# Performance work log

Measured on AMD Instinct MI355X. Metric: run time of the kernel, lower is better.

## Reference

```python
import jax, jax.numpy as jnp
import numpy as np

N_NODES = 50000
N_EDGES = 800000
D = 128
E_DIM = 32
N_LAYERS = 4
BN_EPS = 1e-5


def setup_inputs() -> dict:
    key = jax.random.key(0)
    ks = jax.random.split(key, 9)
    return {
        "x": jax.random.normal(ks[0], (N_NODES, D), dtype=jnp.float32),
        "edge_attr": jax.random.normal(ks[1], (N_EDGES, E_DIM), dtype=jnp.float32),
        "edge_index": jax.random.randint(ks[2], (2, N_EDGES), 0, N_NODES, dtype=jnp.int64),
        "W_edge": jax.random.normal(ks[3], (N_LAYERS, E_DIM, D), dtype=jnp.float32) * 0.1,
        "b_edge": jnp.zeros((N_LAYERS, D), dtype=jnp.float32),
        "W1": jax.random.normal(ks[4], (N_LAYERS, D, D), dtype=jnp.float32) * 0.1,
        "b1": jnp.zeros((N_LAYERS, D), dtype=jnp.float32),
        "W2": jax.random.normal(ks[5], (N_LAYERS, D, D), dtype=jnp.float32) * 0.1,
        "b2": jnp.zeros((N_LAYERS, D), dtype=jnp.float32),
        "gamma": jnp.ones((N_LAYERS, D), dtype=jnp.float32),
        "beta": jnp.zeros((N_LAYERS, D), dtype=jnp.float32),
    }


def reference(x, edge_attr, edge_index, W_edge, b_edge, W1, b1, W2, b2, gamma, beta):
    src, dst = edge_index[0], edge_index[1]
    n = x.shape[0]
    for i in range(N_LAYERS):
        # GINEConv: message = ReLU(x_src + Lin(edge_attr)); scatter-add to dst
        e = edge_attr @ W_edge[i] + b_edge[i]            # [E, D]
        m = jax.nn.relu(x[src] + e)                      # [E, D]
        agg = jax.ops.segment_sum(m, dst, num_segments=n)  # [N, D]
        h = x + agg                                      # (1+eps)*x, eps=0
        # 2-layer MLP
        h = jax.nn.relu(h @ W1[i] + b1[i]) @ W2[i] + b2[i]
        # BatchNorm (training-mode batch stats, biased var) + ReLU; dropout off
        mean = h.mean(axis=0)
        var = h.var(axis=0)
        h = (h - mean) * jax.lax.rsqrt(var + BN_EPS) * gamma[i] + beta[i]
        x = jax.nn.relu(h)
    return x
```

## Files before the change

### kernel.cpp

```cpp
#include <hip/hip_runtime.h>

#define NN 50000
#define NE 800000
#define DD 128
#define ED 32
#define NL 4
#define BN_EPS 1e-5f
#define SCAN_B 1024
#define NB ((NN + SCAN_B - 1) / SCAN_B)
#define EB 128
#define MR 32

typedef __attribute__((ext_vector_type(8))) short bf16x8;
typedef __attribute__((ext_vector_type(4))) float f32x4;

__device__ __forceinline__ unsigned short f2bf(float f) {
    unsigned u = __float_as_uint(f);
    u += 0x7fffu + ((u >> 16) & 1u);
    return (unsigned short)(u >> 16);
}
__device__ __forceinline__ float bf2f(unsigned short h) {
    return __uint_as_float((unsigned)h << 16);
}

__global__ __launch_bounds__(256) void hist_kernel(
    const int* __restrict__ edst, int* __restrict__ deg)
{
    const int e = blockIdx.x * 256 + threadIdx.x;
    if (e < NE) atomicAdd(&deg[edst[e]], 1);
}

__global__ __launch_bounds__(256) void scan1_kernel(
    const int* __restrict__ deg, int* __restrict__ rowptr, int* __restrict__ bsum)
{
    __shared__ int sh[256];
    const int t = threadIdx.x, b = blockIdx.x;
    const int base = b * SCAN_B + t * 4;
    int v[4];
#pragma unroll
    for (int j = 0; j < 4; ++j) {
        const int idx = base + j;
        v[j] = (idx < NN) ? deg[idx] : 0;
    }
    sh[t] = v[0] + v[1] + v[2] + v[3];
    __syncthreads();
    for (int off = 1; off < 256; off <<= 1) {
        const int val = (t >= off) ? sh[t - off] : 0;
        __syncthreads();
        sh[t] += val;
        __syncthreads();
    }
    int p = (t == 0) ? 0 : sh[t - 1];
#pragma unroll
    for (int j = 0; j < 4; ++j) {
        const int idx = base + j;
        if (idx < NN) rowptr[idx] = p;
        p += v[j];
    }
    if (t == 255) bsum[b] = sh[255];
}

__global__ void scan2_kernel(int* __restrict__ bsum)
{
    if (threadIdx.x == 0) {
        int acc = 0;
        for (int i = 0; i < NB; ++i) { const int v = bsum[i]; bsum[i] = acc; acc += v; }
    }
}

__global__ __launch_bounds__(256) void scan3_kernel(
    int* __restrict__ rowptr, int* __restrict__ cursor, const int* __restrict__ bsum)
{
    const int idx = blockIdx.x * 256 + threadIdx.x;
    if (idx < NN) {
        const int v = rowptr[idx] + bsum[idx / SCAN_B];
        rowptr[idx] = v;
        cursor[idx] = v;
    }
    if (idx == 0) rowptr[NN] = NE;
}

__global__ __launch_bounds__(256) void scatter_idx_kernel(
    const int* __restrict__ edst, int* __restrict__ cursor, int* __restrict__ eid_perm)
{
    const int e = blockIdx.x * 256 + threadIdx.x;
    if (e < NE) {
        const int pos = atomicAdd(&cursor[edst[e]], 1);
        eid_perm[pos] = e;
    }
}

__global__ __launch_bounds__(256) void sdea_kernel(
    const int* __restrict__ eid_perm, const int* __restrict__ esrc,
    const int* __restrict__ edst, const float* __restrict__ ea,
    int2* __restrict__ sd_perm, unsigned short* __restrict__ ea_bf)
{
    const int tid = blockIdx.x * 256 + threadIdx.x;
    const int pos = tid >> 3, j = tid & 7;
    if (pos < NE) {
        const int e = eid_perm[pos];
        if (j == 0) sd_perm[pos] = make_int2(esrc[e], edst[e]);
        const float4 v = *(const float4*)&ea[(size_t)e * ED + j * 4];
        uint2 p;
        p.x = (unsigned)f2bf(v.x) | ((unsigned)f2bf(v.y) << 16);
        p.y = (unsigned)f2bf(v.z) | ((unsigned)f2bf(v.w) << 16);
        *(uint2*)&ea_bf[(size_t)pos * ED + j * 4] = p;
    }
    if (tid == 0) sd_perm[NE] = make_int2(0, -1);
}

__global__ __launch_bounds__(256) void x0conv_kernel(
    const float* __restrict__ x0, unsigned short* __restrict__ xbf)
{
    const size_t i = ((size_t)blockIdx.x * 256 + threadIdx.x) * 8;
    if (i >= (size_t)NN * DD) return;
    const float4 a = *(const float4*)&x0[i];
    const float4 b = *(const float4*)&x0[i + 4];
    uint4 o;
    o.x = (unsigned)f2bf(a.x) | ((unsigned)f2bf(a.y) << 16);
    o.y = (unsigned)f2bf(a.z) | ((unsigned)f2bf(a.w) << 16);
    o.z = (unsigned)f2bf(b.x) | ((unsigned)f2bf(b.y) << 16);
    o.w = (unsigned)f2bf(b.z) | ((unsigned)f2bf(b.w) << 16);
    *(uint4*)&xbf[i] = o;
}

__global__ __launch_bounds__(256) void wconv_kernel(
    const float* __restrict__ We, unsigned short* __restrict__ wtb)
{
    const int tid = blockIdx.x * 256 + threadIdx.x;
    if (tid < NL * DD * ED) {
        const int l = tid / (DD * ED);
        const int r = tid % (DD * ED);
        const int c = r / ED, k = r % ED;
        wtb[tid] = f2bf(We[(size_t)l * ED * DD + k * DD + c]);
    }
}

__global__ __launch_bounds__(256) void w12conv_kernel(
    const float* __restrict__ W1, const float* __restrict__ W2,
    unsigned short* __restrict__ w1t, unsigned short* __restrict__ w2t)
{
    const int tid = blockIdx.x * 256 + threadIdx.x;
    if (tid < NL * DD * DD) {
        const int l = tid / (DD * DD);
        const int r = tid % (DD * DD);
        const int n = r / DD, k = r % DD;
        const size_t s = (size_t)l * DD * DD + k * DD + n;
        w1t[tid] = f2bf(W1[s]);
        w2t[tid] = f2bf(W2[s]);
    }
}

__global__ __launch_bounds__(256, 5) void edge_mfma_kernel(
    const unsigned short* __restrict__ xbf,
    const unsigned short* __restrict__ eab,
    const int2* __restrict__ sd_perm,
    const unsigned short* __restrict__ wtb,
    const float* __restrict__ be,
    float* __restrict__ agg)
{
    __shared__ unsigned short msgl[EB * 128];
    const int t = threadIdx.x;
    const int wv = t >> 6, ln = t & 63;
    const int l15 = ln & 15, kb = ln >> 4;

    const int nwg = NE / EB;
    const int q = nwg >> 3, r = nwg & 7;
    const int xcd = blockIdx.x & 7, seq = blockIdx.x >> 3;
    const int wg = (xcd < r ? xcd * (q + 1) : r * (q + 1) + (xcd - r) * q) + seq;
    const int e0 = wg * EB;

    const int c0 = (2 * wv + 0) * 16 + l15;
    const int c1 = (2 * wv + 1) * 16 + l15;
    const bf16x8 bfr0 = *(const bf16x8*)&wtb[c0 * ED + kb * 8];
    const bf16x8 bfr1 = *(const bf16x8*)&wtb[c1 * ED + kb * 8];
    const float bv0 = be[c0], bv1 = be[c1];

#pragma unroll
    for (int eg = 0; eg < EB / 16; ++eg) {
        const int edge = eg * 16 + l15;
        const bf16x8 afr = *(const bf16x8*)&eab[(size_t)(e0 + edge) * ED + kb * 8];
        f32x4 z = {0.f, 0.f, 0.f, 0.f};
        const f32x4 d0 = __builtin_amdgcn_mfma_f32_16x16x32_bf16(afr, bfr0, z, 0, 0, 0);
        const f32x4 d1 = __builtin_amdgcn_mfma_f32_16x16x32_bf16(afr, bfr1, z, 0, 0, 0);
#pragma unroll
        for (int j = 0; j < 4; ++j) {
            const int mrow = eg * 16 + kb * 4 + j;
            const int sw = ((mrow >> 2) & 3) << 3;
            const int i0 = (((c0 >> 1) ^ sw) << 1) | (c0 & 1);
            const int i1 = (((c1 >> 1) ^ sw) << 1) | (c1 & 1);
            msgl[mrow * 128 + i0] = f2bf(d0[j] + bv0);
            msgl[mrow * 128 + i1] = f2bf(d1[j] + bv1);
        }
    }
    __syncthreads();

    const int lbase = wv * 32;
    const int2* sdp = &sd_perm[e0 + lbase];
    const int c2 = ln * 2;
    float2 acc = {0.f, 0.f};
    int seg_start = 0;
#pragma unroll 1
    for (int g = 0; g < 2; ++g) {
        const int gb = g * 16;
        int4 pr[8];
#pragma unroll
        for (int q2 = 0; q2 < 8; ++q2)
            pr[q2] = *(const int4*)&sdp[gb + 2 * q2];
        int srcs[16], dsts[17];
#pragma unroll
        for (int q2 = 0; q2 < 8; ++q2) {
            srcs[2 * q2] = pr[q2].x; srcs[2 * q2 + 1] = pr[q2].z;
            dsts[2 * q2] = pr[q2].y; dsts[2 * q2 + 1] = pr[q2].w;
        }
        dsts[16] = sdp[gb + 16].y;
        float2 xv[16];
#pragma unroll
        for (int q2 = 0; q2 < 16; ++q2) {
            const unsigned xu = *(const unsigned*)&xbf[(size_t)srcs[q2] * DD + c2];
            xv[q2].x = __uint_as_float(xu << 16);
            xv[q2].y = __uint_as_float(xu & 0xffff0000u);
        }
#pragma unroll
        for (int q2 = 0; q2 < 16; ++q2) {
            const int i = gb + q2;
            const int dw = ln ^ (((i >> 2) & 3) << 3);
            const unsigned mm = *(const unsigned*)&msgl[(lbase + i) * 128 + dw * 2];
            const float mlo = __uint_as_float(mm << 16);
            const float mhi = __uint_as_float(mm & 0xffff0000u);
            acc.x += fmaxf(xv[q2].x + mlo, 0.f);
            acc.y += fmaxf(xv[q2].y + mhi, 0.f);
            if (i == 31 || dsts[q2 + 1] != dsts[q2]) {
                float* ap = &agg[(size_t)dsts[q2] * DD + c2];
                if (seg_start > 0 && i < 31) {
                    *(float2*)ap = acc;
                } else {
                    unsafeAtomicAdd(ap + 0, acc.x);
                    unsafeAtomicAdd(ap + 1, acc.y);
                }
                acc.x = 0.f; acc.y = 0.f;
                seg_start = i + 1;
            }
        }
    }
}

__global__ __launch_bounds__(256, 5) void mlp_mfma_kernel(
    const unsigned short* __restrict__ xbf, const float* __restrict__ agg,
    float* __restrict__ h2out,
    const unsigned short* __restrict__ w1t,
    const unsigned short* __restrict__ w2t,
    const float* __restrict__ b1, const float* __restrict__ b2,
    float* __restrict__ bns)
{
    __shared__ unsigned short ah[MR * 128];
    __shared__ unsigned short al[MR * 128];
    __shared__ unsigned short bh[MR * 128];
    const int t = threadIdx.x;
    const int wv = t >> 6, ln = t & 63, l15 = ln & 15, kb = ln >> 4;
    const int r0 = blockIdx.x * MR;

#pragma unroll
    for (int p = 0; p < 2; ++p) {
        const int row = p * 16 + (t >> 4);
        const int gc = t & 15;
        const int grow = r0 + row;
        float v[8] = {0.f, 0.f, 0.f, 0.f, 0.f, 0.f, 0.f, 0.f};
        if (grow < NN) {
            const size_t g = (size_t)grow * DD + gc * 8;
            const uint4 xu = *(const uint4*)&xbf[g];
            const float4 ga = *(const float4*)&agg[g];
            const float4 gb4 = *(const float4*)&agg[g + 4];
            v[0] = __uint_as_float(xu.x << 16)          + ga.x;
            v[1] = __uint_as_float(xu.x & 0xffff0000u)  + ga.y;
            v[2] = __uint_as_float(xu.y << 16)          + ga.z;
            v[3] = __uint_as_float(xu.y & 0xffff0000u)  + ga.w;
            v[4] = __uint_as_float(xu.z << 16)          + gb4.x;
            v[5] = __uint_as_float(xu.z & 0xffff0000u)  + gb4.y;
            v[6] = __uint_as_float(xu.w << 16)          + gb4.z;
            v[7] = __uint_as_float(xu.w & 0xffff0000u)  + gb4.w;
        }
        unsigned hiw[4], low[4];
#pragma unroll
        for (int j = 0; j < 4; ++j) {
            const unsigned short h0 = f2bf(v[2 * j]);
            const unsigned short h1 = f2bf(v[2 * j + 1]);
            const unsigned short q0 = f2bf(v[2 * j] - bf2f(h0));
            const unsigned short q1 = f2bf(v[2 * j + 1] - bf2f(h1));
            hiw[j] = (unsigned)h0 | ((unsigned)h1 << 16);
            low[j] = (unsigned)q0 | ((unsigned)q1 << 16);
        }
        const int off = row * 128 + (gc ^ (row & 7)) * 8;
        *(uint4*)&ah[off] = *(uint4*)hiw;
        *(uint4*)&al[off] = *(uint4*)low;
    }

    bf16x8 w1f[2][4];
#pragma unroll
    for (int nt = 0; nt < 2; ++nt) {
        const int n = wv * 32 + nt * 16 + l15;
#pragma unroll
        for (int ks = 0; ks < 4; ++ks)
            w1f[nt][ks] = *(const bf16x8*)&w1t[n * DD + ks * 32 + kb * 8];
    }
    const int cA = wv * 32 + l15, cB = wv * 32 + 16 + l15;
    const float b1v[2] = {b1[cA], b1[cB]};
    const float b2v[2] = {b2[cA], b2[cB]};
    __syncthreads();

    f32x4 acc[2][2];
#pragma unroll
    for (int mt = 0; mt < 2; ++mt)
#pragma unroll
        for (int nt = 0; nt < 2; ++nt)
            acc[mt][nt] = (f32x4){0.f, 0.f, 0.f, 0.f};
#pragma unroll
    for (int ks = 0; ks < 4; ++ks) {
#pragma unroll
        for (int mt = 0; mt < 2; ++mt) {
            const int row = mt * 16 + l15;
            const int off = row * 128 + ((ks * 4 + kb) ^ (row & 7)) * 8;
            const bf16x8 afh = *(const bf16x8*)&ah[off];
            const bf16x8 afl = *(const bf16x8*)&al[off];
#pragma unroll
            for (int nt = 0; nt < 2; ++nt) {
                acc[mt][nt] = __builtin_amdgcn_mfma_f32_16x16x32_bf16(afh, w1f[nt][ks], acc[mt][nt], 0, 0, 0);
                acc[mt][nt] = __builtin_amdgcn_mfma_f32_16x16x32_bf16(afl, w1f[nt][ks], acc[mt][nt], 0, 0, 0);
            }
        }
    }

#pragma unroll
    for (int mt = 0; mt < 2; ++mt) {
#pragma unroll
        for (int nt = 0; nt < 2; ++nt) {
            const int col = wv * 32 + nt * 16 + l15;
#pragma unroll
            for (int j = 0; j < 4; ++j) {
                const int row = mt * 16 + kb * 4 + j;
                const float v = fmaxf(acc[mt][nt][j] + b1v[nt], 0.f);
                const int off = row * 128 + ((col >> 3) ^ (row & 7)) * 8 + (col & 7);
                bh[off] = f2bf(v);
            }
        }
    }

    bf16x8 w2f[2][4];
#pragma unroll
    for (int nt = 0; nt < 2; ++nt) {
        const int n = wv * 32 + nt * 16 + l15;
#pragma unroll
        for (int ks = 0; ks < 4; ++ks)
            w2f[nt][ks] = *(const bf16x8*)&w2t[n * DD + ks * 32 + kb * 8];
    }
    __syncthreads();

#pragma unroll
    for (int mt = 0; mt < 2; ++mt)
#pragma unroll
        for (int nt = 0; nt < 2; ++nt)
            acc[mt][nt] = (f32x4){0.f, 0.f, 0.f, 0.f};
#pragma unroll
    for (int ks = 0; ks < 4; ++ks) {
#pragma unroll
        for (int mt = 0; mt < 2; ++mt) {
            const int row = mt * 16 + l15;
            const int off = row * 128 + ((ks * 4 + kb) ^ (row & 7)) * 8;
            const bf16x8 afh = *(const bf16x8*)&bh[off];
#pragma unroll
            for (int nt = 0; nt < 2; ++nt)
                acc[mt][nt] = __builtin_amdgcn_mfma_f32_16x16x32_bf16(afh, w2f[nt][ks], acc[mt][nt], 0, 0, 0);
        }
    }

    float ps[2] = {0.f, 0.f}, pq[2] = {0.f, 0.f};
#pragma unroll
    for (int mt = 0; mt < 2; ++mt) {
#pragma unroll
        for (int nt = 0; nt < 2; ++nt) {
            const int col = wv * 32 + nt * 16 + l15;
#pragma unroll
            for (int j = 0; j < 4; ++j) {
                const int row = r0 + mt * 16 + kb * 4 + j;
                const float v = acc[mt][nt][j] + b2v[nt];
                if (row < NN) {
                    h2out[(size_t)row * DD + col] = v;
                    ps[nt] += v;
                    pq[nt] += v * v;
                }
            }
        }
    }
#pragma unroll
    for (int nt = 0; nt < 2; ++nt) {
        ps[nt] += __shfl_xor(ps[nt], 16);
        ps[nt] += __shfl_xor(ps[nt], 32);
        pq[nt] += __shfl_xor(pq[nt], 16);
        pq[nt] += __shfl_xor(pq[nt], 32);
    }
    if (kb == 0) {
#pragma unroll
        for (int nt = 0; nt < 2; ++nt) {
            const int col = wv * 32 + nt * 16 + l15;
            unsafeAtomicAdd(&bns[col], ps[nt]);
            unsafeAtomicAdd(&bns[DD + col], pq[nt]);
        }
    }
}

__global__ __launch_bounds__(256) void bn_apply_bf16(
    float* __restrict__ h2, const float* __restrict__ bns,
    const float* __restrict__ gamma, const float* __restrict__ beta,
    unsigned short* __restrict__ xout)
{
    const size_t i = ((size_t)blockIdx.x * 256 + threadIdx.x) * 4;
    if (i >= (size_t)NN * DD) return;
    const int c4 = (int)(i & 127);
    const float4 hv = *(const float4*)&h2[i];
    const float4 sv = *(const float4*)&bns[c4];
    const float4 qv = *(const float4*)&bns[DD + c4];
    const float4 gv = *(const float4*)&gamma[c4];
    const float4 bv = *(const float4*)&beta[c4];
    const float inv_n = 1.f / (float)NN;
    float o0, o1, o2, o3;
    { const float m = sv.x * inv_n; const float var = qv.x * inv_n - m * m;
      o0 = fmaxf((hv.x - m) * __frsqrt_rn(var + BN_EPS) * gv.x + bv.x, 0.f); }
    { const float m = sv.y * inv_n; const float var = qv.y * inv_n - m * m;
      o1 = fmaxf((hv.y - m) * __frsqrt_rn(var + BN_EPS) * gv.y + bv.y, 0.f); }
    { const float m = sv.z * inv_n; const float var = qv.z * inv_n - m * m;
      o2 = fmaxf((hv.z - m) * __frsqrt_rn(var + BN_EPS) * gv.z + bv.z, 0.f); }
    { const float m = sv.w * inv_n; const float var = qv.w * inv_n - m * m;
      o3 = fmaxf((hv.w - m) * __frsqrt_rn(var + BN_EPS) * gv.w + bv.w, 0.f); }
    uint2 o;
    o.x = (unsigned)f2bf(o0) | ((unsigned)f2bf(o1) << 16);
    o.y = (unsigned)f2bf(o2) | ((unsigned)f2bf(o3) << 16);
    *(uint2*)&xout[i] = o;
    *(float4*)&h2[i] = (float4){0.f, 0.f, 0.f, 0.f};
}

__global__ __launch_bounds__(256) void bn_apply_f32(
    const float* __restrict__ h2, const float* __restrict__ bns,
    const float* __restrict__ gamma, const float* __restrict__ beta,
    float* __restrict__ xout)
{
    const size_t i = ((size_t)blockIdx.x * 256 + threadIdx.x) * 4;
    if (i >= (size_t)NN * DD) return;
    const int c4 = (int)(i & 127);
    const float4 hv = *(const float4*)&h2[i];
    const float4 sv = *(const float4*)&bns[c4];
    const float4 qv = *(const float4*)&bns[DD + c4];
    const float4 gv = *(const float4*)&gamma[c4];
    const float4 bv = *(const float4*)&beta[c4];
    const float inv_n = 1.f / (float)NN;
    float4 ov;
    { const float m = sv.x * inv_n; const float var = qv.x * inv_n - m * m;
      ov.x = fmaxf((hv.x - m) * __frsqrt_rn(var + BN_EPS) * gv.x + bv.x, 0.f); }
    { const float m = sv.y * inv_n; const float var = qv.y * inv_n - m * m;
      ov.y = fmaxf((hv.y - m) * __frsqrt_rn(var + BN_EPS) * gv.y + bv.y, 0.f); }
    { const float m = sv.z * inv_n; const float var = qv.z * inv_n - m * m;
      ov.z = fmaxf((hv.z - m) * __frsqrt_rn(var + BN_EPS) * gv.z + bv.z, 0.f); }
    { const float m = sv.w * inv_n; const float var = qv.w * inv_n - m * m;
      ov.w = fmaxf((hv.w - m) * __frsqrt_rn(var + BN_EPS) * gv.w + bv.w, 0.f); }
    *(float4*)&xout[i] = ov;
}

extern "C" void kernel_launch(void* const* d_in, const int* in_sizes, int n_in,
                              void* d_out, int out_size, void* d_ws, size_t ws_size,
                              hipStream_t stream) {
    const float* x0    = (const float*)d_in[0];
    const float* ea    = (const float*)d_in[1];
    const int*   eidx  = (const int*)d_in[2];
    const float* We    = (const float*)d_in[3];
    const float* be    = (const float*)d_in[4];
    const float* W1    = (const float*)d_in[5];
    const float* b1    = (const float*)d_in[6];
    const float* W2    = (const float*)d_in[7];
    const float* b2    = (const float*)d_in[8];
    const float* gamma = (const float*)d_in[9];
    const float* beta  = (const float*)d_in[10];
    float* out = (float*)d_out;
    float* ws  = (float*)d_ws;

    float* agg = ws;
    float* bns = agg + (size_t)NN * DD;
    int* deg      = (int*)(bns + NL * 256);
    int* rowptr   = deg + 50000;
    int* cursor   = rowptr + 50004;
    int* bsum     = cursor + 50000;
    int2* sd_perm = (int2*)(bsum + 64);
    int* eid_perm = (int*)(sd_perm + NE + 2);
    unsigned short* ea_bf = (unsigned short*)(eid_perm + NE);
    unsigned short* wt_bf = ea_bf + (size_t)NE * ED;
    unsigned short* w1t   = wt_bf + (size_t)NL * DD * ED;
    unsigned short* w2t   = w1t + (size_t)NL * DD * DD;
    unsigned short* xbf   = w2t + (size_t)NL * DD * DD;

    const int* esrc = eidx;
    const int* edst = eidx + NE;

    hipMemsetAsync(deg, 0, NN * sizeof(int), stream);
    hipMemsetAsync(bns, 0, NL * 256 * sizeof(float), stream);
    hipMemsetAsync(agg, 0, (size_t)NN * DD * sizeof(float), stream);
    hist_kernel<<<(NE + 255) / 256, 256, 0, stream>>>(edst, deg);
    scan1_kernel<<<NB, 256, 0, stream>>>(deg, rowptr, bsum);
    scan2_kernel<<<1, 64, 0, stream>>>(bsum);
    scan3_kernel<<<(NN + 255) / 256, 256, 0, stream>>>(rowptr, cursor, bsum);
    scatter_idx_kernel<<<(NE + 255) / 256, 256, 0, stream>>>(edst, cursor, eid_perm);
    sdea_kernel<<<((size_t)NE * 8 + 255) / 256, 256, 0, stream>>>(
        eid_perm, esrc, edst, ea, sd_perm, ea_bf);
    x0conv_kernel<<<((NN * DD / 8) + 255) / 256, 256, 0, stream>>>(x0, xbf);
    wconv_kernel<<<(NL * DD * ED + 255) / 256, 256, 0, stream>>>(We, wt_bf);
    w12conv_kernel<<<(NL * DD * DD + 255) / 256, 256, 0, stream>>>(W1, W2, w1t, w2t);

    for (int l = 0; l < NL; ++l) {
        edge_mfma_kernel<<<NE / EB, 256, 0, stream>>>(
            xbf, ea_bf, sd_perm,
            wt_bf + (size_t)l * DD * ED, be + (size_t)l * DD, agg);
        mlp_mfma_kernel<<<(NN + MR - 1) / MR, 256, 0, stream>>>(
            xbf, agg, agg,
            w1t + (size_t)l * DD * DD, w2t + (size_t)l * DD * DD,
            b1 + (size_t)l * DD, b2 + (size_t)l * DD, bns + l * 256);
        if (l < NL - 1) {
            bn_apply_bf16<<<(NN * DD / 4 + 255) / 256, 256, 0, stream>>>(
                agg, bns + l * 256, gamma + (size_t)l * DD, beta + (size_t)l * DD, xbf);
        } else {
            bn_apply_f32<<<(NN * DD / 4 + 255) / 256, 256, 0, stream>>>(
                agg, bns + l * 256, gamma + (size_t)l * DD, beta + (size_t)l * DD, out);
        }
    }
}
```

Measured before the change: 655.4 us.

## Pack src/dst into 16-bit pairs and reuse histogram ranks for CSR placement

```diff
diff --git a/kernel.cpp b/kernel.cpp
--- a/kernel.cpp
+++ b/kernel.cpp
@@ -23,11 +23,11 @@
     return __uint_as_float((unsigned)h << 16);
 }
 
-__global__ __launch_bounds__(256) void hist_kernel(
-    const int* __restrict__ edst, int* __restrict__ deg)
+__global__ __launch_bounds__(256) void hist_rank_kernel(
+    const int* __restrict__ edst, int* __restrict__ deg, int* __restrict__ rank)
 {
     const int e = blockIdx.x * 256 + threadIdx.x;
-    if (e < NE) atomicAdd(&deg[edst[e]], 1);
+    if (e < NE) rank[e] = atomicAdd(&deg[edst[e]], 1);
 }
 
 __global__ __launch_bounds__(256) void scan1_kernel(
@@ -69,44 +69,39 @@
 }
 
 __global__ __launch_bounds__(256) void scan3_kernel(
-    int* __restrict__ rowptr, int* __restrict__ cursor, const int* __restrict__ bsum)
+    int* __restrict__ rowptr, const int* __restrict__ bsum)
 {
     const int idx = blockIdx.x * 256 + threadIdx.x;
-    if (idx < NN) {
-        const int v = rowptr[idx] + bsum[idx / SCAN_B];
-        rowptr[idx] = v;
-        cursor[idx] = v;
-    }
+    if (idx < NN) rowptr[idx] += bsum[idx / SCAN_B];
     if (idx == 0) rowptr[NN] = NE;
 }
 
-__global__ __launch_bounds__(256) void scatter_idx_kernel(
-    const int* __restrict__ edst, int* __restrict__ cursor, int* __restrict__ eid_perm)
+__global__ __launch_bounds__(256) void place_kernel(
+    const int* __restrict__ edst, const int* __restrict__ rowptr,
+    const int* __restrict__ rank, int* __restrict__ eid_perm)
 {
     const int e = blockIdx.x * 256 + threadIdx.x;
-    if (e < NE) {
-        const int pos = atomicAdd(&cursor[edst[e]], 1);
-        eid_perm[pos] = e;
-    }
+    if (e < NE) eid_perm[rowptr[edst[e]] + rank[e]] = e;
 }
 
 __global__ __launch_bounds__(256) void sdea_kernel(
     const int* __restrict__ eid_perm, const int* __restrict__ esrc,
     const int* __restrict__ edst, const float* __restrict__ ea,
-    int2* __restrict__ sd_perm, unsigned short* __restrict__ ea_bf)
+    unsigned* __restrict__ sd_pk, unsigned short* __restrict__ ea_bf)
 {
     const int tid = blockIdx.x * 256 + threadIdx.x;
     const int pos = tid >> 3, j = tid & 7;
     if (pos < NE) {
         const int e = eid_perm[pos];
-        if (j == 0) sd_perm[pos] = make_int2(esrc[e], edst[e]);
+        if (j == 0)
+            sd_pk[pos] = (unsigned)esrc[e] | ((unsigned)edst[e] << 16);
         const float4 v = *(const float4*)&ea[(size_t)e * ED + j * 4];
         uint2 p;
         p.x = (unsigned)f2bf(v.x) | ((unsigned)f2bf(v.y) << 16);
         p.y = (unsigned)f2bf(v.z) | ((unsigned)f2bf(v.w) << 16);
         *(uint2*)&ea_bf[(size_t)pos * ED + j * 4] = p;
     }
-    if (tid == 0) sd_perm[NE] = make_int2(0, -1);
+    if (tid == 0) sd_pk[NE] = 0xFFFF0000u;
 }
 
 __global__ __launch_bounds__(256) void x0conv_kernel(
@@ -154,7 +149,7 @@
 __global__ __launch_bounds__(256, 5) void edge_mfma_kernel(
     const unsigned short* __restrict__ xbf,
     const unsigned short* __restrict__ eab,
-    const int2* __restrict__ sd_perm,
+    const unsigned* __restrict__ sd_pk,
     const unsigned short* __restrict__ wtb,
     const float* __restrict__ be,
     float* __restrict__ agg)
@@ -196,28 +191,29 @@
     __syncthreads();
 
     const int lbase = wv * 32;
-    const int2* sdp = &sd_perm[e0 + lbase];
+    const unsigned* sdp = &sd_pk[e0 + lbase];
     const int c2 = ln * 2;
     float2 acc = {0.f, 0.f};
     int seg_start = 0;
 #pragma unroll 1
     for (int g = 0; g < 2; ++g) {
         const int gb = g * 16;
-        int4 pr[8];
-#pragma unroll
-        for (int q2 = 0; q2 < 8; ++q2)
-            pr[q2] = *(const int4*)&sdp[gb + 2 * q2];
-        int srcs[16], dsts[17];
-#pragma unroll
-        for (int q2 = 0; q2 < 8; ++q2) {
-            srcs[2 * q2] = pr[q2].x; srcs[2 * q2 + 1] = pr[q2].z;
-            dsts[2 * q2] = pr[q2].y; dsts[2 * q2 + 1] = pr[q2].w;
-        }
-        dsts[16] = sdp[gb + 16].y;
+        uint4 pr[4];
+#pragma unroll
+        for (int q2 = 0; q2 < 4; ++q2)
+            pr[q2] = *(const uint4*)&sdp[gb + 4 * q2];
+        unsigned pk[17];
+#pragma unroll
+        for (int q2 = 0; q2 < 4; ++q2) {
+            pk[4 * q2 + 0] = pr[q2].x; pk[4 * q2 + 1] = pr[q2].y;
+            pk[4 * q2 + 2] = pr[q2].z; pk[4 * q2 + 3] = pr[q2].w;
+        }
+        pk[16] = sdp[gb + 16];
         float2 xv[16];
 #pragma unroll
         for (int q2 = 0; q2 < 16; ++q2) {
-            const unsigned xu = *(const unsigned*)&xbf[(size_t)srcs[q2] * DD + c2];
+            const unsigned src = pk[q2] & 0xFFFFu;
+            const unsigned xu = *(const unsigned*)&xbf[(size_t)src * DD + c2];
             xv[q2].x = __uint_as_float(xu << 16);
             xv[q2].y = __uint_as_float(xu & 0xffff0000u);
         }
@@ -230,8 +226,9 @@
             const float mhi = __uint_as_float(mm & 0xffff0000u);
             acc.x += fmaxf(xv[q2].x + mlo, 0.f);
             acc.y += fmaxf(xv[q2].y + mhi, 0.f);
-            if (i == 31 || dsts[q2 + 1] != dsts[q2]) {
-                float* ap = &agg[(size_t)dsts[q2] * DD + c2];
+            const unsigned d_cur = pk[q2] >> 16;
+            if (i == 31 || (pk[q2 + 1] >> 16) != d_cur) {
+                float* ap = &agg[(size_t)d_cur * DD + c2];
                 if (seg_start > 0 && i < 31) {
                     *(float2*)ap = acc;
                 } else {
@@ -485,11 +482,11 @@
     float* bns = agg + (size_t)NN * DD;
     int* deg      = (int*)(bns + NL * 256);
     int* rowptr   = deg + 50000;
-    int* cursor   = rowptr + 50004;
-    int* bsum     = cursor + 50000;
-    int2* sd_perm = (int2*)(bsum + 64);
-    int* eid_perm = (int*)(sd_perm + NE + 2);
-    unsigned short* ea_bf = (unsigned short*)(eid_perm + NE);
+    int* bsum     = rowptr + 50004;
+    int* rank     = bsum + 64;
+    int* eid_perm = rank + NE;
+    unsigned* sd_pk = (unsigned*)(eid_perm + NE);
+    unsigned short* ea_bf = (unsigned short*)(sd_pk + NE + 4);
     unsigned short* wt_bf = ea_bf + (size_t)NE * ED;
     unsigned short* w1t   = wt_bf + (size_t)NL * DD * ED;
     unsigned short* w2t   = w1t + (size_t)NL * DD * DD;
@@ -501,20 +498,20 @@
     hipMemsetAsync(deg, 0, NN * sizeof(int), stream);
     hipMemsetAsync(bns, 0, NL * 256 * sizeof(float), stream);
     hipMemsetAsync(agg, 0, (size_t)NN * DD * sizeof(float), stream);
-    hist_kernel<<<(NE + 255) / 256, 256, 0, stream>>>(edst, deg);
+    hist_rank_kernel<<<(NE + 255) / 256, 256, 0, stream>>>(edst, deg, rank);
     scan1_kernel<<<NB, 256, 0, stream>>>(deg, rowptr, bsum);
     scan2_kernel<<<1, 64, 0, stream>>>(bsum);
-    scan3_kernel<<<(NN + 255) / 256, 256, 0, stream>>>(rowptr, cursor, bsum);
-    scatter_idx_kernel<<<(NE + 255) / 256, 256, 0, stream>>>(edst, cursor, eid_perm);
+    scan3_kernel<<<(NN + 255) / 256, 256, 0, stream>>>(rowptr, bsum);
+    place_kernel<<<(NE + 255) / 256, 256, 0, stream>>>(edst, rowptr, rank, eid_perm);
     sdea_kernel<<<((size_t)NE * 8 + 255) / 256, 256, 0, stream>>>(
-        eid_perm, esrc, edst, ea, sd_perm, ea_bf);
+        eid_perm, esrc, edst, ea, sd_pk, ea_bf);
     x0conv_kernel<<<((NN * DD / 8) + 255) / 256, 256, 0, stream>>>(x0, xbf);
     wconv_kernel<<<(NL * DD * ED + 255) / 256, 256, 0, stream>>>(We, wt_bf);
     w12conv_kernel<<<(NL * DD * DD + 255) / 256, 256, 0, stream>>>(W1, W2, w1t, w2t);
 
     for (int l = 0; l < NL; ++l) {
         edge_mfma_kernel<<<NE / EB, 256, 0, stream>>>(
-            xbf, ea_bf, sd_perm,
+            xbf, ea_bf, sd_pk,
             wt_bf + (size_t)l * DD * ED, be + (size_t)l * DD, agg);
         mlp_mfma_kernel<<<(NN + MR - 1) / MR, 256, 0, stream>>>(
             xbf, agg, agg,
```

Result: faster. 610.9 us (-6.8%).
